# Performance work log

Measured on AMD Instinct MI355X. Metric: run time of the kernel, lower is better.

Reference implementation:

```python
import jax, jax.numpy as jnp
import numpy as np

TWO_PI = 2.0 * np.pi


def setup_inputs() -> dict:
    key = jax.random.key(0)
    k1, k2 = jax.random.split(key)
    B, N, F = 1, 4096, 4096
    query_points = jax.random.normal(k1, (B, N, 3), dtype=jnp.float32)
    face_coord = jax.random.normal(k2, (B, F, 3, 3), dtype=jnp.float32)
    return {"query_points": query_points, "face_coord": face_coord}


def _winding(query_points, face_coord):
    # query_points: [B, N, 3]; face_coord: [B, F, 3, 3]
    # Per-pair vectors from query point to each triangle vertex: [B, N, F, 3]
    qp = query_points[:, :, None, :]  # [B, N, 1, 3]
    a = face_coord[:, None, :, 0, :] - qp
    b = face_coord[:, None, :, 1, :] - qp
    c = face_coord[:, None, :, 2, :] - qp

    det = jnp.sum(a * jnp.cross(b, c), axis=-1)          # [B, N, F]
    na = jnp.linalg.norm(a, axis=-1)
    nb = jnp.linalg.norm(b, axis=-1)
    nc = jnp.linalg.norm(c, axis=-1)
    ab = jnp.sum(a * b, axis=-1)
    bc = jnp.sum(b * c, axis=-1)
    ac = jnp.sum(a * c, axis=-1)

    denom = na * nb * nc + bc * na + ac * nb + ab * nc
    solid_angle_2 = jnp.arctan2(det, denom)              # [B, N, F]
    # Sum solid angles over all faces, normalize by 2*pi -> winding number/occupancy
    return jnp.sum(solid_angle_2, axis=-1) / TWO_PI      # [B, N]


def reference(query_points, face_coord):
    return _winding(query_points, face_coord)
```

## Files before the change

### kernel.cpp

```cpp
#include <hip/hip_runtime.h>
#include <math.h>

#define N_Q 4096
#define N_F 4096
#define NBLK 512
#define QPW 2
#define TF 256
#define NT (N_F / TF)
#define REC 12
#define INV_2PI 0.15915494309189535f

__device__ __forceinline__ float fast_atan2f(float y, float x) {
    const float pi   = 3.14159265358979f;
    const float pi_2 = 1.57079632679490f;
    float ax = fabsf(x), ay = fabsf(y);
    float mx = fmaxf(ax, ay), mn = fminf(ax, ay);
    mx = fmaxf(mx, 1e-30f);
    float t = mn * __builtin_amdgcn_rcpf(mx);
    float s = t * t;
    float p =              -0.0117212f;
    p = fmaf(p, s,  0.05265332f);
    p = fmaf(p, s, -0.11643287f);
    p = fmaf(p, s,  0.19354346f);
    p = fmaf(p, s, -0.33262347f);
    p = fmaf(p, s,  0.99997726f);
    float r = p * t;
    r = (ay > ax) ? (pi_2 - r) : r;
    r = (x < 0.0f) ? (pi - r) : r;
    return copysignf(r, y);
}

__device__ __forceinline__ void merge_angle(
    float y1, float x1, float y2, float x2,
    float& ym, float& xm, float& w)
{
    ym = fmaf(y1, x2, y2 * x1);
    xm = fmaf(-y1, y2, x1 * x2);
    const float c = copysignf(1.0f, y1) + copysignf(1.0f, y2);
    w += (ym * c < 0.0f) ? 0.5f * c : 0.0f;
}

__device__ __forceinline__ void raw_dn(
    float qx, float qy, float qz,
    float v0, float v1, float v2, float v3, float v4,
    float v5, float v6, float v7, float v8,
    float& det, float& den)
{
    const float ax = v0 - qx, ay = v1 - qy, az = v2 - qz;
    const float bx = v3 - qx, by = v4 - qy, bz = v5 - qz;
    const float cx = v6 - qx, cy = v7 - qy, cz = v8 - qz;

    const float ux = fmaf(by, cz, -bz * cy);
    const float uy = fmaf(bz, cx, -bx * cz);
    const float uz = fmaf(bx, cy, -by * cx);
    det = fmaf(ax, ux, fmaf(ay, uy, az * uz));

    const float na = __builtin_amdgcn_sqrtf(fmaf(ax, ax, fmaf(ay, ay, az * az)));
    const float nb = __builtin_amdgcn_sqrtf(fmaf(bx, bx, fmaf(by, by, bz * bz)));
    const float nc = __builtin_amdgcn_sqrtf(fmaf(cx, cx, fmaf(cy, cy, cz * cz)));

    const float ab = fmaf(ax, bx, fmaf(ay, by, az * bz));
    const float bc = fmaf(bx, cx, fmaf(by, cy, bz * cz));
    const float ac = fmaf(ax, cx, fmaf(ay, cy, az * cz));

    den = fmaf(na * nb, nc, fmaf(bc, na, fmaf(ac, nb, ab * nc)));
}

__global__ __launch_bounds__(256) void winding_kernel(
    const float* __restrict__ qp,
    const float* __restrict__ fc,
    float* __restrict__ out)
{
    __shared__ __align__(16) float buf[2][TF * REC];
    __shared__ float aux[2][TF];

    const int tid  = threadIdx.x;
    const int lane = tid & 63;
    const int wid  = tid >> 6;
    const int q0   = blockIdx.x * 8 + wid * QPW;
    const int q1   = q0 + 1;

    const float q0x = qp[q0*3+0], q0y = qp[q0*3+1], q0z = qp[q0*3+2];
    const float q1x = qp[q1*3+0], q1y = qp[q1*3+1], q1z = qp[q1*3+2];

    {
        const float* src = fc + (size_t)tid * 9;
        float r[9];
        #pragma unroll
        for (int k = 0; k < 9; ++k) r[k] = src[k];
        float4* b4 = (float4*)buf[0];
        b4[tid*3+0] = make_float4(r[0], r[1], r[2], r[3]);
        b4[tid*3+1] = make_float4(r[4], r[5], r[6], r[7]);
        aux[0][tid] = r[8];
    }
    __syncthreads();

    float s0 = 0.0f, w0 = 0.0f, s1 = 0.0f, w1 = 0.0f;

    for (int t = 0; t < NT; ++t) {
        const int cur = t & 1;

        float r[9];
        if (t + 1 < NT) {
            const float* src = fc + ((size_t)(t + 1) * TF + tid) * 9;
            #pragma unroll
            for (int k = 0; k < 9; ++k) r[k] = src[k];
        }

        const float4* b4 = (const float4*)buf[cur];
        float d0[4], n0[4], d1[4], n1[4];
        #pragma unroll
        for (int i = 0; i < 4; ++i) {
            const int fi = lane + (i << 6);
            const float4 p0 = b4[fi*3+0];
            const float4 p1 = b4[fi*3+1];
            const float v8 = aux[cur][fi];
            raw_dn(q0x,q0y,q0z, p0.x,p0.y,p0.z,p0.w, p1.x,p1.y,p1.z,p1.w, v8,
                   d0[i], n0[i]);
            raw_dn(q1x,q1y,q1z, p0.x,p0.y,p0.z,p0.w, p1.x,p1.y,p1.z,p1.w, v8,
                   d1[i], n1[i]);
        }

        {
            float ya,xa,yb,xb,Y,X;
            merge_angle(d0[0],n0[0], d0[1],n0[1], ya,xa, w0);
            merge_angle(d0[2],n0[2], d0[3],n0[3], yb,xb, w0);
            merge_angle(ya,xa, yb,xb, Y,X, w0);
            s0 += fast_atan2f(Y, X);
        }
        {
            float ya,xa,yb,xb,Y,X;
            merge_angle(d1[0],n1[0], d1[1],n1[1], ya,xa, w1);
            merge_angle(d1[2],n1[2], d1[3],n1[3], yb,xb, w1);
            merge_angle(ya,xa, yb,xb, Y,X, w1);
            s1 += fast_atan2f(Y, X);
        }

        if (t + 1 < NT) {
            __syncthreads();
            float4* wb = (float4*)buf[cur ^ 1];
            wb[tid*3+0] = make_float4(r[0], r[1], r[2], r[3]);
            wb[tid*3+1] = make_float4(r[4], r[5], r[6], r[7]);
            aux[cur ^ 1][tid] = r[8];
            __syncthreads();
        }
    }

    #pragma unroll
    for (int m = 1; m < 64; m <<= 1) {
        s0 += __shfl_xor(s0, m);
        w0 += __shfl_xor(w0, m);
        s1 += __shfl_xor(s1, m);
        w1 += __shfl_xor(w1, m);
    }
    if (lane == 0) {
        out[q0] = fmaf(s0, INV_2PI, w0);
        out[q1] = fmaf(s1, INV_2PI, w1);
    }
}

extern "C" void kernel_launch(void* const* d_in, const int* in_sizes, int n_in,
                              void* d_out, int out_size, void* d_ws, size_t ws_size,
                              hipStream_t stream) {
    const float* qp = (const float*)d_in[0];
    const float* fc = (const float*)d_in[1];
    float* out = (float*)d_out;

    winding_kernel<<<dim3(NBLK), dim3(256), 0, stream>>>(qp, fc, out);
}
```

Measured before the change: 30.36 us.

## Assign one query per wavefront, double grid size, use single barrier per tile

Each wavefront now handles one query point instead of two, and the grid doubles to 1024 blocks of four queries each. This gives more parallelism and lower register pressure, but each face tile loaded into LDS is now reused by half as many queries, so global and LDS traffic per query doubles. The two barriers around the double-buffer write become one barrier after the write. That is safe because writes go to the other buffer, which was last read in the previous iteration before that iteration's barrier.

```diff
diff --git a/kernel.cpp b/kernel.cpp
--- a/kernel.cpp
+++ b/kernel.cpp
@@ -3,11 +3,9 @@
 
 #define N_Q 4096
 #define N_F 4096
-#define NBLK 512
-#define QPW 2
+#define NBLK 1024
 #define TF 256
 #define NT (N_F / TF)
-#define REC 12
 #define INV_2PI 0.15915494309189535f
 
 __device__ __forceinline__ float fast_atan2f(float y, float x) {
@@ -71,17 +69,15 @@
     const float* __restrict__ fc,
     float* __restrict__ out)
 {
-    __shared__ __align__(16) float buf[2][TF * REC];
+    __shared__ __align__(16) float buf[2][TF * 12];
     __shared__ float aux[2][TF];
 
     const int tid  = threadIdx.x;
     const int lane = tid & 63;
     const int wid  = tid >> 6;
-    const int q0   = blockIdx.x * 8 + wid * QPW;
-    const int q1   = q0 + 1;
+    const int q    = blockIdx.x * 4 + wid;
 
-    const float q0x = qp[q0*3+0], q0y = qp[q0*3+1], q0z = qp[q0*3+2];
-    const float q1x = qp[q1*3+0], q1y = qp[q1*3+1], q1z = qp[q1*3+2];
+    const float qx = qp[q*3+0], qy = qp[q*3+1], qz = qp[q*3+2];
 
     {
         const float* src = fc + (size_t)tid * 9;
@@ -95,7 +91,7 @@
     }
     __syncthreads();
 
-    float s0 = 0.0f, w0 = 0.0f, s1 = 0.0f, w1 = 0.0f;
+    float s = 0.0f, w = 0.0f;
 
     for (int t = 0; t < NT; ++t) {
         const int cur = t & 1;
@@ -108,55 +104,38 @@
         }
 
         const float4* b4 = (const float4*)buf[cur];
-        float d0[4], n0[4], d1[4], n1[4];
+        float d[4], n[4];
         #pragma unroll
         for (int i = 0; i < 4; ++i) {
             const int fi = lane + (i << 6);
             const float4 p0 = b4[fi*3+0];
             const float4 p1 = b4[fi*3+1];
             const float v8 = aux[cur][fi];
-            raw_dn(q0x,q0y,q0z, p0.x,p0.y,p0.z,p0.w, p1.x,p1.y,p1.z,p1.w, v8,
-                   d0[i], n0[i]);
-            raw_dn(q1x,q1y,q1z, p0.x,p0.y,p0.z,p0.w, p1.x,p1.y,p1.z,p1.w, v8,
-                   d1[i], n1[i]);
+            raw_dn(qx,qy,qz, p0.x,p0.y,p0.z,p0.w, p1.x,p1.y,p1.z,p1.w, v8,
+                   d[i], n[i]);
         }
 
-        {
-            float ya,xa,yb,xb,Y,X;
-            merge_angle(d0[0],n0[0], d0[1],n0[1], ya,xa, w0);
-            merge_angle(d0[2],n0[2], d0[3],n0[3], yb,xb, w0);
-            merge_angle(ya,xa, yb,xb, Y,X, w0);
-            s0 += fast_atan2f(Y, X);
-        }
-        {
-            float ya,xa,yb,xb,Y,X;
-            merge_angle(d1[0],n1[0], d1[1],n1[1], ya,xa, w1);
-            merge_angle(d1[2],n1[2], d1[3],n1[3], yb,xb, w1);
-            merge_angle(ya,xa, yb,xb, Y,X, w1);
-            s1 += fast_atan2f(Y, X);
-        }
+        float ya,xa,yb,xb,Y,X;
+        merge_angle(d[0],n[0], d[1],n[1], ya,xa, w);
+        merge_angle(d[2],n[2], d[3],n[3], yb,xb, w);
+        merge_angle(ya,xa, yb,xb, Y,X, w);
+        s += fast_atan2f(Y, X);
 
         if (t + 1 < NT) {
-            __syncthreads();
             float4* wb = (float4*)buf[cur ^ 1];
             wb[tid*3+0] = make_float4(r[0], r[1], r[2], r[3]);
             wb[tid*3+1] = make_float4(r[4], r[5], r[6], r[7]);
             aux[cur ^ 1][tid] = r[8];
-            __syncthreads();
         }
+        __syncthreads();
     }
 
     #pragma unroll
     for (int m = 1; m < 64; m <<= 1) {
-        s0 += __shfl_xor(s0, m);
-        w0 += __shfl_xor(w0, m);
-        s1 += __shfl_xor(s1, m);
-        w1 += __shfl_xor(w1, m);
+        s += __shfl_xor(s, m);
+        w += __shfl_xor(w, m);
     }
-    if (lane == 0) {
-        out[q0] = fmaf(s0, INV_2PI, w0);
-        out[q1] = fmaf(s1, INV_2PI, w1);
-    }
+    if (lane == 0) out[q] = fmaf(s, INV_2PI, w);
 }
 
 extern "C" void kernel_launch(void* const* d_in, const int* in_sizes, int n_in,
```

Result: slower. 33.12 us (+9.1%).
